# Kernel optimization log

Hardware: AMD Instinct MI355X
Metric: run time of the kernel (lower is better)

Reference implementation:

```python
import jax, jax.numpy as jnp
import numpy as np

T, B, D = 200, 1024, 128
T_OBS = 140
L = 20       # rec_dims: encoder latent per mean/std
LAT = 32     # latents: generative latent dim
GRU_U = 200  # gru_units
UNITS = 100  # hidden units of ODE-func / z0 nets


def _lin(key, fan_in, fan_out):
    return jax.random.normal(key, (fan_in, fan_out), jnp.float32) / jnp.sqrt(jnp.float32(fan_in))


def setup_inputs() -> dict:
    key = jax.random.key(0)
    ks = jax.random.split(key, 20)
    gin = 2 * L + 2 * D  # GRU input: (mean,std) + (data,mask)
    inp = {
        "truth": jax.random.normal(ks[0], (T, B, D), jnp.float32),
        "t": jnp.arange(T, dtype=jnp.float32),
        "obs_idx": jnp.sort(jax.random.randint(ks[1], (T_OBS,), 0, T)),
        "eps": jax.random.normal(ks[2], (B, LAT), jnp.float32),
        # encoder ODE func (rec_layers=1 hidden layer of UNITS)
        "enc_w1": _lin(ks[3], L, UNITS), "enc_b1": jnp.zeros(UNITS, jnp.float32),
        "enc_w2": _lin(ks[4], UNITS, L), "enc_b2": jnp.zeros(L, jnp.float32),
        # GRU unit: update / reset / new-state nets
        "gru_uw1": _lin(ks[5], gin, GRU_U), "gru_ub1": jnp.zeros(GRU_U, jnp.float32),
        "gru_uw2": _lin(ks[6], GRU_U, 2 * L), "gru_ub2": jnp.zeros(2 * L, jnp.float32),
        "gru_rw1": _lin(ks[7], gin, GRU_U), "gru_rb1": jnp.zeros(GRU_U, jnp.float32),
        "gru_rw2": _lin(ks[8], GRU_U, 2 * L), "gru_rb2": jnp.zeros(2 * L, jnp.float32),
        "gru_nw1": _lin(ks[9], gin, GRU_U), "gru_nb1": jnp.zeros(GRU_U, jnp.float32),
        "gru_nw2": _lin(ks[10], GRU_U, 2 * L), "gru_nb2": jnp.zeros(2 * L, jnp.float32),
        # transform hidden -> z0 (mean,std)
        "z0_w1": _lin(ks[11], 2 * L, UNITS), "z0_b1": jnp.zeros(UNITS, jnp.float32),
        "z0_w2": _lin(ks[12], UNITS, 2 * LAT), "z0_b2": jnp.zeros(2 * LAT, jnp.float32),
        # decoder ODE func (gen_layers=2 hidden layers of UNITS)
        "dec_w1": _lin(ks[13], LAT, UNITS), "dec_b1": jnp.zeros(UNITS, jnp.float32),
        "dec_w2": _lin(ks[14], UNITS, UNITS), "dec_b2": jnp.zeros(UNITS, jnp.float32),
        "dec_w3": _lin(ks[15], UNITS, LAT), "dec_b3": jnp.zeros(LAT, jnp.float32),
        # readout latent -> data space
        "out_w": _lin(ks[16], LAT, D), "out_b": jnp.zeros(D, jnp.float32),
    }
    return inp


def _rk4(f, y, dt):
    k1 = f(y)
    k2 = f(y + 0.5 * dt * k1)
    k3 = f(y + 0.5 * dt * k2)
    k4 = f(y + dt * k3)
    return y + (dt / 6.0) * (k1 + 2.0 * k2 + 2.0 * k3 + k4)


def reference(truth, t, obs_idx, eps,
              enc_w1, enc_b1, enc_w2, enc_b2,
              gru_uw1, gru_ub1, gru_uw2, gru_ub2,
              gru_rw1, gru_rb1, gru_rw2, gru_rb2,
              gru_nw1, gru_nb1, gru_nw2, gru_nb2,
              z0_w1, z0_b1, z0_w2, z0_b2,
              dec_w1, dec_b1, dec_w2, dec_b2, dec_w3, dec_b3,
              out_w, out_b):
    enc_f = lambda y: jnp.tanh(y @ enc_w1 + enc_b1) @ enc_w2 + enc_b2
    dec_f = lambda z: (jnp.tanh(jnp.tanh(z @ dec_w1 + dec_b1) @ dec_w2 + dec_b2)
                       @ dec_w3 + dec_b3)

    # ----- ODE-RNN encoder, run_backwards=True over observed timesteps -----
    x_obs = truth[obs_idx][::-1]                     # [To, B, D], time-reversed
    t_obs = t[obs_idx][::-1]
    dts = jnp.concatenate([jnp.zeros(1, t.dtype), jnp.diff(t_obs)])  # <=0 steps

    def enc_step(carry, inp):
        ym, ys = carry                               # [B,L] each
        x, dt = inp
        ym = _rk4(enc_f, ym, dt)                     # evolve mean between obs
        xm = jnp.concatenate([x, jnp.ones_like(x)], -1)   # data + mask(=1)
        y = jnp.concatenate([ym, ys], -1)            # [B, 2L]
        yc = jnp.concatenate([y, xm], -1)            # [B, 2L+2D]
        u = jax.nn.sigmoid(jnp.tanh(yc @ gru_uw1 + gru_ub1) @ gru_uw2 + gru_ub2)
        r = jax.nn.sigmoid(jnp.tanh(yc @ gru_rw1 + gru_rb1) @ gru_rw2 + gru_rb2)
        nc = jnp.concatenate([y * r, xm], -1)
        ns = jnp.tanh(nc @ gru_nw1 + gru_nb1) @ gru_nw2 + gru_nb2
        nm, nsd = ns[:, :L], jnp.abs(ns[:, L:])
        new_y = (1.0 - u) * jnp.concatenate([nm, nsd], -1) + u * y
        return (new_y[:, :L], new_y[:, L:]), None

    nb = truth.shape[1]
    init = (jnp.zeros((nb, L), truth.dtype), jnp.zeros((nb, L), truth.dtype))
    (ym, ys), _ = jax.lax.scan(enc_step, init, (x_obs, dts))

    # ----- z0 posterior and sample (n_traj_samples=1) -----
    h = jnp.tanh(jnp.concatenate([ym, ys], -1) @ z0_w1 + z0_b1) @ z0_w2 + z0_b2
    z0_mean, z0_std = h[:, :LAT], jnp.abs(h[:, LAT:])
    z = z0_mean + eps * z0_std                       # [B, LAT]

    # ----- Neural ODE decoder over time_steps_to_predict = t -----
    def dec_step(zc, dt):
        zn = _rk4(dec_f, zc, dt)
        return zn, zn
    _, zs = jax.lax.scan(dec_step, z, jnp.diff(t))
    sol = jnp.concatenate([z[None], zs], 0)          # [T, B, LAT]

    out = sol @ out_w + out_b                        # [T, B, D]
    return jnp.transpose(out, (1, 0, 2))[None]       # [1, B, T, D]
```

## Files before the change

### kernel.cpp

```cpp
#include <hip/hip_runtime.h>
#include <math.h>

#define BB 1024
#define DD 128
#define NWG 256
#define CH 28
#define NCH 5

#define WS_WPACK 0
#define WS_B1E   81920
#define WS_W1Y   82560
#define WS_Y     106560
#define WS_Z     147520
#define WS_HPRE  180288
#define WS_SOL   180288

__device__ __forceinline__ float bcast(float v, int lane) {
    return __uint_as_float(__builtin_amdgcn_readlane(__float_as_uint(v), lane));
}

__device__ __forceinline__ float tanh_fast(float x) {
    const float t = __builtin_amdgcn_exp2f(x * 2.88539008177793f);
    return 1.f - 2.f * __builtin_amdgcn_rcpf(t + 1.f);
}
__device__ __forceinline__ float sigm_fast(float x) {
    const float t = __builtin_amdgcn_exp2f(x * -1.4426950408889634f);
    return __builtin_amdgcn_rcpf(1.f + t);
}

__global__ __launch_bounds__(256) void prep_kernel(
    const float* __restrict__ uw1, const float* __restrict__ ub1,
    const float* __restrict__ rw1, const float* __restrict__ rb1,
    const float* __restrict__ nw1, const float* __restrict__ nb1,
    float* __restrict__ ws)
{
    int tid = blockIdx.x * blockDim.x + threadIdx.x;
    int nth = gridDim.x * blockDim.x;
    for (int idx = tid; idx < 128 * 640; idx += nth) {
        int k = idx / 640, j = idx - k * 640;
        float v = 0.f;
        if (j < 600) {
            int g = j / 200, jj = j - g * 200;
            const float* w1 = (g == 0) ? uw1 : (g == 1) ? rw1 : nw1;
            v = w1[(40 + k) * 200 + jj];
        }
        ws[WS_WPACK + idx] = v;
    }
    for (int j = tid; j < 640; j += nth) {
        float s = 0.f;
        if (j < 600) {
            int g = j / 200, jj = j - g * 200;
            const float* w1 = (g == 0) ? uw1 : (g == 1) ? rw1 : nw1;
            const float* b1 = (g == 0) ? ub1 : (g == 1) ? rb1 : nb1;
            s = b1[jj];
            for (int k = 168; k < 296; ++k) s += w1[k * 200 + jj];
        }
        ws[WS_B1E + j] = s;
    }
    for (int idx = tid; idx < 40 * 600; idx += nth) {
        int k = idx / 600, j = idx - k * 600;
        int g = j / 200, jj = j - g * 200;
        const float* w1 = (g == 0) ? uw1 : (g == 1) ? rw1 : nw1;
        ws[WS_W1Y + idx] = w1[k * 200 + jj];
    }
}

__global__ __launch_bounds__(256) void hpre_gemm(
    const float* __restrict__ truth, const int* __restrict__ obs_idx,
    const float* __restrict__ ws, float* __restrict__ hpre, int s0)
{
    __shared__ float sx[64][68];
    __shared__ float sw[64][132];
    const int t0 = threadIdx.x;
    const int jt = blockIdx.x % 5;
    const int bt = (blockIdx.x / 5) % 16;
    const int sl = blockIdx.x / 80;
    const int oi = obs_idx[139 - (s0 + sl)];
    const int b0 = bt * 64;
    const float* wpack = ws + WS_WPACK;
    const float* b1e   = ws + WS_B1E;

    const int jj  = t0 & 15;
    const int bb4 = t0 >> 4;
    float acc[8][4];
#pragma unroll
    for (int m = 0; m < 8; ++m)
#pragma unroll
        for (int q = 0; q < 4; ++q) acc[m][q] = 0.f;

    for (int kh = 0; kh < 2; ++kh) {
        __syncthreads();
        for (int i = t0; i < 64 * 16; i += 256) {
            int bb = i >> 4, kq = i & 15;
            const float4 v = *(const float4*)&truth[((size_t)oi * BB + b0 + bb) * DD + kh * 64 + kq * 4];
            *(float4*)&sx[bb][kq * 4] = v;
        }
        for (int i = t0; i < 64 * 32; i += 256) {
            int kk = i >> 5, jq = i & 31;
            const float4 v = *(const float4*)&wpack[(kh * 64 + kk) * 640 + jt * 128 + jq * 4];
            *(float4*)&sw[kk][jq * 4] = v;
        }
        __syncthreads();
#pragma unroll 4
        for (int k = 0; k < 64; ++k) {
            float xv[4], wv[8];
#pragma unroll
            for (int q = 0; q < 4; ++q) xv[q] = sx[bb4 * 4 + q][k];
#pragma unroll
            for (int m = 0; m < 8; ++m) wv[m] = sw[k][jj + 16 * m];
#pragma unroll
            for (int m = 0; m < 8; ++m)
#pragma unroll
                for (int q = 0; q < 4; ++q) acc[m][q] += wv[m] * xv[q];
        }
    }
    const int bblk = bt * 16 + bb4;
#pragma unroll
    for (int m = 0; m < 8; ++m) {
        int j = jt * 128 + jj + 16 * m;
        if (j < 600) {
            float be = b1e[j];
#pragma unroll
            for (int q = 0; q < 4; ++q)
                hpre[(size_t)((sl * 256 + bblk) * 4 + q) * 600 + j] = acc[m][q] + be;
        }
    }
}

__global__ __launch_bounds__(256, 1) void enc_chunk(
    const float* __restrict__ tg, const int* __restrict__ obs_idx,
    const float* __restrict__ eps,
    const float* __restrict__ ew1, const float* __restrict__ eb1,
    const float* __restrict__ ew2, const float* __restrict__ eb2,
    const float* __restrict__ uw2, const float* __restrict__ ub2,
    const float* __restrict__ rw2, const float* __restrict__ rb2,
    const float* __restrict__ nw2, const float* __restrict__ nb2,
    const float* __restrict__ z0w1, const float* __restrict__ z0b1,
    const float* __restrict__ z0w2, const float* __restrict__ z0b2,
    float* __restrict__ ws, int s0)
{
    __shared__ float s_t[200];
    __shared__ int   s_oi[140];
    __shared__ __align__(16) float s_y[40][4];
    __shared__ __align__(16) float s_ytmp[20][4];
    __shared__ float s_kacc[20][4];
    __shared__ __align__(16) float s_hid[4][104];
    __shared__ float s_pe[20][4][2];
    __shared__ __align__(16) float s_ew1t[100 * 20];
    __shared__ __align__(16) float s_w2n[40 * 212];
    __shared__ __align__(16) float s_hur[4][416];
    __shared__ __align__(16) float s_hn[4][208];
    __shared__ float s_pw[80][4][4];
    __shared__ float s_pn[40][4][4];
    __shared__ float s_u[40][4];
    __shared__ __align__(16) float s_yr[40][4];
    __shared__ float s_z0o[4][64];

    const int t0 = threadIdx.x;
    const int bblk = blockIdx.x;
    const int b0 = bblk * 4;
    const float* hpre = ws + WS_HPRE;

    float rgy[3][40];
    float rew2h[52];
    float rw2q[2][52];
    float eb1_r = 0.f, eb2_r = 0.f, bur_r = 0.f, bn_r = 0.f;

    if (t0 < 200) {
#pragma unroll
        for (int g = 0; g < 3; ++g)
#pragma unroll
            for (int k = 0; k < 40; ++k)
                rgy[g][k] = ws[WS_W1Y + k * 600 + g * 200 + t0];
    }
    if (t0 < 100) eb1_r = eb1[t0];
    if (t0 < 160) {
        const int c2 = t0 % 20, kh = t0 / 80;
#pragma unroll
        for (int i = 0; i < 52; ++i) {
            const int row = kh * 52 + i;
            rew2h[i] = (row < 100) ? ew2[row * 20 + c2] : 0.f;
        }
    }
    if (t0 < 80) eb2_r = eb2[t0 % 20];
    if (t0 < 160) {
        const int p = t0 % 20, g = (t0 / 20) % 2, kq = t0 / 40;
        const float* w2 = g ? rw2 : uw2;
#pragma unroll
        for (int j = 0; j < 2; ++j)
#pragma unroll
            for (int i = 0; i < 52; ++i) {
                const int row = kq * 52 + i;
                rw2q[j][i] = (row < 200) ? w2[row * 40 + p + 20 * j] : 0.f;
            }
        bur_r = ((t0 % 80) < 40) ? ub2[t0 % 80] : rb2[(t0 % 80) - 40];
        bn_r = nb2[t0 % 40];
    }

    for (int i = t0; i < 2000; i += 256) { int k = i / 100, c = i % 100; s_ew1t[c * 20 + k] = ew1[i]; }
    for (int i = t0; i < 40 * 212; i += 256) { int o = i / 212, k = i % 212; s_w2n[i] = (k < 200) ? nw2[k * 40 + o] : 0.f; }
    for (int i = t0; i < 200; i += 256) s_t[i] = tg[i];
    for (int i = t0; i < 140; i += 256) s_oi[i] = obs_idx[i];
    if (t0 < 160) { int k = t0 % 40, b = t0 / 40; s_y[k][b] = s0 ? ws[WS_Y + k * 1024 + b0 + b] : 0.f; }
    if (t0 < 4) {
#pragma unroll
        for (int i = 0; i < 4; ++i) s_hid[t0][100 + i] = 0.f;
#pragma unroll
        for (int i = 0; i < 8; ++i) { s_hur[t0][200 + i] = 0.f; s_hur[t0][408 + i] = 0.f; s_hn[t0][200 + i] = 0.f; }
    }
    __syncthreads();

    for (int sl = 0; sl < CH; ++sl) {
        const int s = s0 + sl;
        const int oi = s_oi[139 - s];
        const float dt = (s == 0) ? 0.f : (s_t[oi] - s_t[s_oi[140 - s]]);

        float hpu[4], hpr[4], hpn[4];
        if (t0 < 200) {
#pragma unroll
            for (int q = 0; q < 4; ++q) {
                const size_t r = (size_t)((sl * 256 + bblk) * 4 + q) * 600;
                hpu[q] = hpre[r + t0];
                hpr[q] = hpre[r + 200 + t0];
                hpn[q] = hpre[r + 400 + t0];
            }
        }

#pragma unroll 1
        for (int e = 0; e < 4; ++e) {
            if (t0 < 100) {
                const int c = t0;
                float a[4] = {eb1_r, eb1_r, eb1_r, eb1_r};
#pragma unroll
                for (int i = 0; i < 5; ++i) {
                    const float4 wv = *(const float4*)&s_ew1t[c * 20 + 4 * i];
                    const float wk[4] = {wv.x, wv.y, wv.z, wv.w};
#pragma unroll
                    for (int kk = 0; kk < 4; ++kk) {
                        const int k = 4 * i + kk;
                        const float4 yv = (e == 0) ? *(const float4*)&s_y[k][0]
                                                   : *(const float4*)&s_ytmp[k][0];
                        a[0] += wk[kk] * yv.x; a[1] += wk[kk] * yv.y;
                        a[2] += wk[kk] * yv.z; a[3] += wk[kk] * yv.w;
                    }
                }
#pragma unroll
                for (int b = 0; b < 4; ++b) s_hid[b][c] = tanh_fast(a[b]);
            }
            __syncthreads();
            if (t0 < 160) {
                const int c2 = t0 % 20, b = (t0 / 20) % 4, kh = t0 / 80;
                float acc = 0.f;
#pragma unroll
                for (int i = 0; i < 13; ++i) {
                    const float4 hv = *(const float4*)&s_hid[b][kh * 52 + 4 * i];
                    acc += hv.x * rew2h[4 * i] + hv.y * rew2h[4 * i + 1]
                         + hv.z * rew2h[4 * i + 2] + hv.w * rew2h[4 * i + 3];
                }
                s_pe[c2][b][kh] = acc;
            }
            __syncthreads();
            if (t0 < 80) {
                const int c2 = t0 % 20, b = t0 / 20;
                const float kv = eb2_r + s_pe[c2][b][0] + s_pe[c2][b][1];
                const float y0 = s_y[c2][b];
                if (e == 0)      { s_kacc[c2][b] = kv;        s_ytmp[c2][b] = y0 + 0.5f * dt * kv; }
                else if (e == 1) { s_kacc[c2][b] += 2.f * kv; s_ytmp[c2][b] = y0 + 0.5f * dt * kv; }
                else if (e == 2) { s_kacc[c2][b] += 2.f * kv; s_ytmp[c2][b] = y0 + dt * kv; }
                else             { s_y[c2][b] = y0 + (dt / 6.f) * (s_kacc[c2][b] + kv); }
            }
            __syncthreads();
        }

        if (t0 < 200) {
            float au[4], ar[4];
#pragma unroll
            for (int b = 0; b < 4; ++b) { au[b] = hpu[b]; ar[b] = hpr[b]; }
#pragma unroll
            for (int k = 0; k < 40; ++k) {
                const float4 yv = *(const float4*)&s_y[k][0];
                const float wu = rgy[0][k], wr = rgy[1][k];
                au[0] += wu * yv.x; au[1] += wu * yv.y; au[2] += wu * yv.z; au[3] += wu * yv.w;
                ar[0] += wr * yv.x; ar[1] += wr * yv.y; ar[2] += wr * yv.z; ar[3] += wr * yv.w;
            }
#pragma unroll
            for (int b = 0; b < 4; ++b) {
                s_hur[b][t0] = tanh_fast(au[b]);
                s_hur[b][208 + t0] = tanh_fast(ar[b]);
            }
        }
        __syncthreads();

        if (t0 < 160) {
            const int p = t0 % 20, g = (t0 / 20) % 2, kq = t0 / 40;
            const int goff = g * 208;
            float a1[4] = {0.f, 0.f, 0.f, 0.f}, a2[4] = {0.f, 0.f, 0.f, 0.f};
#pragma unroll
            for (int i = 0; i < 13; ++i) {
                const float wa = rw2q[0][4 * i], wb = rw2q[0][4 * i + 1],
                            wc = rw2q[0][4 * i + 2], wd = rw2q[0][4 * i + 3];
                const float we = rw2q[1][4 * i], wf = rw2q[1][4 * i + 1],
                            wg = rw2q[1][4 * i + 2], wh = rw2q[1][4 * i + 3];
#pragma unroll
                for (int b = 0; b < 4; ++b) {
                    const float4 hv = *(const float4*)&s_hur[b][goff + kq * 52 + 4 * i];
                    a1[b] += hv.x * wa + hv.y * wb + hv.z * wc + hv.w * wd;
                    a2[b] += hv.x * we + hv.y * wf + hv.z * wg + hv.w * wh;
                }
            }
            const int o1 = 40 * g + p, o2 = o1 + 20;
#pragma unroll
            for (int b = 0; b < 4; ++b) { s_pw[o1][b][kq] = a1[b]; s_pw[o2][b][kq] = a2[b]; }
        }
        __syncthreads();

        if (t0 < 160) {
            const int o = t0 % 80, bp = t0 / 80;
#pragma unroll
            for (int j = 0; j < 2; ++j) {
                const int b = 2 * bp + j;
                const float v = bur_r + s_pw[o][b][0] + s_pw[o][b][1] + s_pw[o][b][2] + s_pw[o][b][3];
                const float sg = sigm_fast(v);
                if (o < 40) s_u[o][b] = sg;
                else        s_yr[o - 40][b] = s_y[o - 40][b] * sg;
            }
        }
        __syncthreads();

        if (t0 < 200) {
            float an[4];
#pragma unroll
            for (int b = 0; b < 4; ++b) an[b] = hpn[b];
#pragma unroll
            for (int k = 0; k < 40; ++k) {
                const float4 yv = *(const float4*)&s_yr[k][0];
                const float w = rgy[2][k];
                an[0] += w * yv.x; an[1] += w * yv.y; an[2] += w * yv.z; an[3] += w * yv.w;
            }
#pragma unroll
            for (int b = 0; b < 4; ++b) s_hn[b][t0] = tanh_fast(an[b]);
        }
        __syncthreads();

        if (t0 < 160) {
            const int o = t0 % 40, kq = t0 / 40;
            float an[4] = {0.f, 0.f, 0.f, 0.f};
#pragma unroll
            for (int i = 0; i < 13; ++i) {
                const float4 wv = *(const float4*)&s_w2n[o * 212 + kq * 52 + 4 * i];
#pragma unroll
                for (int b = 0; b < 4; ++b) {
                    const float4 hv = *(const float4*)&s_hn[b][kq * 52 + 4 * i];
                    an[b] += hv.x * wv.x + hv.y * wv.y + hv.z * wv.z + hv.w * wv.w;
                }
            }
#pragma unroll
            for (int b = 0; b < 4; ++b) s_pn[o][b][kq] = an[b];
        }
        __syncthreads();

        if (t0 < 160) {
            const int o = t0 % 40, b = t0 / 40;
            const float v = bn_r + s_pn[o][b][0] + s_pn[o][b][1] + s_pn[o][b][2] + s_pn[o][b][3];
            const float cand = (o < 20) ? v : fabsf(v);
            const float uu = s_u[o][b];
            s_y[o][b] = (1.f - uu) * cand + uu * s_y[o][b];
        }
        __syncthreads();
    }

    if (s0 + CH == 140) {
        if (t0 < 100) {
            const int c = t0;
            float a[4] = {z0b1[c], z0b1[c], z0b1[c], z0b1[c]};
#pragma unroll
            for (int k = 0; k < 40; ++k) {
                const float4 yv = *(const float4*)&s_y[k][0];
                const float w = z0w1[k * 100 + c];
                a[0] += w * yv.x; a[1] += w * yv.y; a[2] += w * yv.z; a[3] += w * yv.w;
            }
#pragma unroll
            for (int b = 0; b < 4; ++b) s_hid[b][c] = tanh_fast(a[b]);
        }
        __syncthreads();
        {
            const int b = t0 / 64, u = t0 % 64;
            float acc = z0b2[u];
#pragma unroll
            for (int i = 0; i < 25; ++i) {
                const float4 hv = *(const float4*)&s_hid[b][4 * i];
                acc += hv.x * z0w2[(4 * i) * 64 + u] + hv.y * z0w2[(4 * i + 1) * 64 + u]
                     + hv.z * z0w2[(4 * i + 2) * 64 + u] + hv.w * z0w2[(4 * i + 3) * 64 + u];
            }
            s_z0o[b][u] = acc;
        }
        __syncthreads();
        if (t0 < 128) {
            const int b = t0 / 32, i = t0 % 32;
            const int gb = b0 + b;
            ws[WS_Z + gb * 32 + i] = s_z0o[b][i] + eps[gb * 32 + i] * fabsf(s_z0o[b][32 + i]);
        }
    }
    if (t0 < 160) {
        const int k = t0 % 40, b = t0 / 40;
        ws[WS_Y + k * 1024 + b0 + b] = s_y[k][b];
    }
}

__global__ __launch_bounds__(128, 2) void dec_kernel(
    const float* __restrict__ tg,
    const float* __restrict__ dw1, const float* __restrict__ db1,
    const float* __restrict__ dw2, const float* __restrict__ db2,
    const float* __restrict__ dw3, const float* __restrict__ db3,
    float* __restrict__ ws)
{
    __shared__ float s_t[200];
    __shared__ float s_p1[2][100];
    __shared__ float s_p2[2][100];
    __shared__ float s_p3[2][32];

    const int t0 = threadIdx.x;
    const int w  = t0 >> 6;
    const int l  = t0 & 63;
    const int batch = blockIdx.x;

    const int c0 = l;
    const int c1 = 64 + l;
    const bool has1 = (l < 36);
    const int j3 = l & 31;

    float rw1a[16], rw1b[16], rw2a[50], rw2b[50], rw3[50];
#pragma unroll
    for (int i = 0; i < 16; ++i) {
        rw1a[i] = dw1[(16 * w + i) * 100 + c0];
        rw1b[i] = has1 ? dw1[(16 * w + i) * 100 + c1] : 0.f;
    }
#pragma unroll
    for (int i = 0; i < 50; ++i) {
        rw2a[i] = dw2[(50 * w + i) * 100 + c0];
        rw2b[i] = has1 ? dw2[(50 * w + i) * 100 + c1] : 0.f;
        rw3[i]  = dw3[(50 * w + i) * 32 + j3];
    }
    const float rb1a = db1[c0];
    const float rb1b = has1 ? db1[c1] : 0.f;
    const float rb2a = db2[c0];
    const float rb2b = has1 ? db2[c1] : 0.f;
    const float rb3  = db3[j3];

    for (int i = t0; i < 200; i += 128) s_t[i] = tg[i];

    float z_r = ws[WS_Z + (size_t)batch * 32 + j3];
    __syncthreads();

    float zs = z_r, ka_r = 0.f;

    for (int s = 0; s < 200; ++s) {
        if (t0 < 32)
            ws[WS_SOL + (size_t)(s * 1024 + batch) * 32 + l] = z_r;
        if (s == 199) break;
        const float dtv = s_t[s + 1] - s_t[s];

#pragma unroll 1
        for (int e = 0; e < 4; ++e) {
            float a0 = 0.f, a1 = 0.f;
            if (w == 0) {
#pragma unroll
                for (int i = 0; i < 16; ++i) {
                    const float sv = bcast(zs, i);
                    a0 += sv * rw1a[i]; a1 += sv * rw1b[i];
                }
            } else {
#pragma unroll
                for (int i = 0; i < 16; ++i) {
                    const float sv = bcast(zs, 16 + i);
                    a0 += sv * rw1a[i]; a1 += sv * rw1b[i];
                }
            }
            s_p1[w][c0] = a0;
            if (has1) s_p1[w][c1] = a1;
            __syncthreads();
            const float h1_0 = tanh_fast(rb1a + a0 + s_p1[w ^ 1][c0]);
            const float h1_1 = has1 ? tanh_fast(rb1b + a1 + s_p1[w ^ 1][c1]) : 0.f;

            float a2 = 0.f, a3 = 0.f;
            if (w == 0) {
#pragma unroll
                for (int i = 0; i < 50; ++i) {
                    const float sv = bcast(h1_0, i);
                    a2 += sv * rw2a[i]; a3 += sv * rw2b[i];
                }
            } else {
#pragma unroll
                for (int i = 0; i < 14; ++i) {
                    const float sv = bcast(h1_0, 50 + i);
                    a2 += sv * rw2a[i]; a3 += sv * rw2b[i];
                }
#pragma unroll
                for (int i = 14; i < 50; ++i) {
                    const float sv = bcast(h1_1, i - 14);
                    a2 += sv * rw2a[i]; a3 += sv * rw2b[i];
                }
            }
            s_p2[w][c0] = a2;
            if (has1) s_p2[w][c1] = a3;
            __syncthreads();
            const float h2_0 = tanh_fast(rb2a + a2 + s_p2[w ^ 1][c0]);
            const float h2_1 = has1 ? tanh_fast(rb2b + a3 + s_p2[w ^ 1][c1]) : 0.f;

            float ap = 0.f;
            if (w == 0) {
#pragma unroll
                for (int i = 0; i < 50; ++i) ap += bcast(h2_0, i) * rw3[i];
            } else {
#pragma unroll
                for (int i = 0; i < 14; ++i) ap += bcast(h2_0, 50 + i) * rw3[i];
#pragma unroll
                for (int i = 14; i < 50; ++i) ap += bcast(h2_1, i - 14) * rw3[i];
            }
            if (l < 32) s_p3[w][l] = ap;
            __syncthreads();
            const float kj = rb3 + s_p3[0][j3] + s_p3[1][j3];

            if (e == 0)      { ka_r = kj;        zs = z_r + 0.5f * dtv * kj; }
            else if (e == 1) { ka_r += 2.f * kj; zs = z_r + 0.5f * dtv * kj; }
            else if (e == 2) { ka_r += 2.f * kj; zs = z_r + dtv * kj; }
            else             { z_r += (dtv / 6.f) * (ka_r + kj); zs = z_r; }
        }
    }
}

__global__ __launch_bounds__(256) void proj_kernel(
    const float* __restrict__ ow, const float* __restrict__ ob,
    const float* __restrict__ ws, float* __restrict__ out)
{
    const int t0 = threadIdx.x;
    const int d = t0 & 127, half = t0 >> 7;
    float rw[32];
#pragma unroll
    for (int k = 0; k < 32; ++k) rw[k] = ow[k * 128 + d];
    const float bo = ob[d];
    const int sb0 = blockIdx.x * 64 + half * 32;
#pragma unroll 2
    for (int m = 0; m < 32; ++m) {
        const int sb = sb0 + m;
        const int s = sb >> 10, b = sb & 1023;
        const float4* zp = (const float4*)&ws[WS_SOL + (size_t)sb * 32];
        float acc = bo;
#pragma unroll
        for (int kq = 0; kq < 8; ++kq) {
            const float4 zv = zp[kq];
            acc += zv.x * rw[4 * kq] + zv.y * rw[4 * kq + 1]
                 + zv.z * rw[4 * kq + 2] + zv.w * rw[4 * kq + 3];
        }
        out[((size_t)b * 200 + s) * 128 + d] = acc;
    }
}

extern "C" void kernel_launch(void* const* d_in, const int* in_sizes, int n_in,
                              void* d_out, int out_size, void* d_ws, size_t ws_size,
                              hipStream_t stream)
{
    const float* truth = (const float*)d_in[0];
    const float* tg    = (const float*)d_in[1];
    const int*   oi    = (const int*)d_in[2];
    const float* eps   = (const float*)d_in[3];
    const float* ew1   = (const float*)d_in[4];
    const float* eb1   = (const float*)d_in[5];
    const float* ew2   = (const float*)d_in[6];
    const float* eb2   = (const float*)d_in[7];
    const float* uw1   = (const float*)d_in[8];
    const float* ub1   = (const float*)d_in[9];
    const float* uw2   = (const float*)d_in[10];
    const float* ub2   = (const float*)d_in[11];
    const float* rw1   = (const float*)d_in[12];
    const float* rb1   = (const float*)d_in[13];
    const float* rw2   = (const float*)d_in[14];
    const float* rb2   = (const float*)d_in[15];
    const float* nw1   = (const float*)d_in[16];
    const float* nb1   = (const float*)d_in[17];
    const float* nw2   = (const float*)d_in[18];
    const float* nb2   = (const float*)d_in[19];
    const float* z0w1  = (const float*)d_in[20];
    const float* z0b1  = (const float*)d_in[21];
    const float* z0w2  = (const float*)d_in[22];
    const float* z0b2  = (const float*)d_in[23];
    const float* dw1   = (const float*)d_in[24];
    const float* db1   = (const float*)d_in[25];
    const float* dw2   = (const float*)d_in[26];
    const float* db2   = (const float*)d_in[27];
    const float* dw3   = (const float*)d_in[28];
    const float* db3   = (const float*)d_in[29];
    const float* ow    = (const float*)d_in[30];
    const float* ob    = (const float*)d_in[31];
    float* ws  = (float*)d_ws;
    float* out = (float*)d_out;

    prep_kernel<<<dim3(120), dim3(256), 0, stream>>>(uw1, ub1, rw1, rb1, nw1, nb1, ws);
    for (int c = 0; c < NCH; ++c) {
        hpre_gemm<<<dim3(CH * 16 * 5), dim3(256), 0, stream>>>(truth, oi, ws, ws + WS_HPRE, c * CH);
        enc_chunk<<<dim3(NWG), dim3(256), 0, stream>>>(
            tg, oi, eps, ew1, eb1, ew2, eb2, uw2, ub2, rw2, rb2, nw2, nb2,
            z0w1, z0b1, z0w2, z0b2, ws, c * CH);
    }
    dec_kernel<<<dim3(1024), dim3(128), 0, stream>>>(tg, dw1, db1, dw2, db2, dw3, db3, ws);
    proj_kernel<<<dim3(3200), dim3(256), 0, stream>>>(ow, ob, ws, out);
}
```

Baseline: 3.800 ms.

## Cut encoder register pressure to allow two workgroups per CU

Raises enc_chunk launch bounds to two workgroups per CU. To fit the register budget, it moves the encoder ODE second-layer weights from per-thread registers into a transposed, padded shared-memory array. It also defers the hpre loads from the top of each step to just before their use. This frees registers for higher occupancy, but adds LDS traffic and exposes global-load latency that was previously hidden behind the RK4 loop.

```diff
diff --git a/kernel.cpp b/kernel.cpp
--- a/kernel.cpp
+++ b/kernel.cpp
@@ -127,7 +127,7 @@
     }
 }
 
-__global__ __launch_bounds__(256, 1) void enc_chunk(
+__global__ __launch_bounds__(256, 2) void enc_chunk(
     const float* __restrict__ tg, const int* __restrict__ obs_idx,
     const float* __restrict__ eps,
     const float* __restrict__ ew1, const float* __restrict__ eb1,
@@ -147,6 +147,7 @@
     __shared__ __align__(16) float s_hid[4][104];
     __shared__ float s_pe[20][4][2];
     __shared__ __align__(16) float s_ew1t[100 * 20];
+    __shared__ __align__(16) float s_ew2t[20 * 108];
     __shared__ __align__(16) float s_w2n[40 * 212];
     __shared__ __align__(16) float s_hur[4][416];
     __shared__ __align__(16) float s_hn[4][208];
@@ -162,7 +163,6 @@
     const float* hpre = ws + WS_HPRE;
 
     float rgy[3][40];
-    float rew2h[52];
     float rw2q[2][52];
     float eb1_r = 0.f, eb2_r = 0.f, bur_r = 0.f, bn_r = 0.f;
 
@@ -174,14 +174,6 @@
                 rgy[g][k] = ws[WS_W1Y + k * 600 + g * 200 + t0];
     }
     if (t0 < 100) eb1_r = eb1[t0];
-    if (t0 < 160) {
-        const int c2 = t0 % 20, kh = t0 / 80;
-#pragma unroll
-        for (int i = 0; i < 52; ++i) {
-            const int row = kh * 52 + i;
-            rew2h[i] = (row < 100) ? ew2[row * 20 + c2] : 0.f;
-        }
-    }
     if (t0 < 80) eb2_r = eb2[t0 % 20];
     if (t0 < 160) {
         const int p = t0 % 20, g = (t0 / 20) % 2, kq = t0 / 40;
@@ -198,6 +190,8 @@
     }
 
     for (int i = t0; i < 2000; i += 256) { int k = i / 100, c = i % 100; s_ew1t[c * 20 + k] = ew1[i]; }
+    for (int i = t0; i < 2000; i += 256) { int row = i / 20, c = i % 20; s_ew2t[c * 108 + row] = ew2[i]; }
+    if (t0 < 160) { int c = t0 % 20, r = 100 + t0 / 20; s_ew2t[c * 108 + r] = 0.f; }
     for (int i = t0; i < 40 * 212; i += 256) { int o = i / 212, k = i % 212; s_w2n[i] = (k < 200) ? nw2[k * 40 + o] : 0.f; }
     for (int i = t0; i < 200; i += 256) s_t[i] = tg[i];
     for (int i = t0; i < 140; i += 256) s_oi[i] = obs_idx[i];
@@ -214,17 +208,6 @@
         const int s = s0 + sl;
         const int oi = s_oi[139 - s];
         const float dt = (s == 0) ? 0.f : (s_t[oi] - s_t[s_oi[140 - s]]);
-
-        float hpu[4], hpr[4], hpn[4];
-        if (t0 < 200) {
-#pragma unroll
-            for (int q = 0; q < 4; ++q) {
-                const size_t r = (size_t)((sl * 256 + bblk) * 4 + q) * 600;
-                hpu[q] = hpre[r + t0];
-                hpr[q] = hpre[r + 200 + t0];
-                hpn[q] = hpre[r + 400 + t0];
-            }
-        }
 
 #pragma unroll 1
         for (int e = 0; e < 4; ++e) {
@@ -250,12 +233,13 @@
             __syncthreads();
             if (t0 < 160) {
                 const int c2 = t0 % 20, b = (t0 / 20) % 4, kh = t0 / 80;
+                const float* wp = &s_ew2t[c2 * 108 + kh * 52];
                 float acc = 0.f;
 #pragma unroll
                 for (int i = 0; i < 13; ++i) {
+                    const float4 wv = *(const float4*)&wp[4 * i];
                     const float4 hv = *(const float4*)&s_hid[b][kh * 52 + 4 * i];
-                    acc += hv.x * rew2h[4 * i] + hv.y * rew2h[4 * i + 1]
-                         + hv.z * rew2h[4 * i + 2] + hv.w * rew2h[4 * i + 3];
+                    acc += hv.x * wv.x + hv.y * wv.y + hv.z * wv.z + hv.w * wv.w;
                 }
                 s_pe[c2][b][kh] = acc;
             }
@@ -275,7 +259,11 @@
         if (t0 < 200) {
             float au[4], ar[4];
 #pragma unroll
-            for (int b = 0; b < 4; ++b) { au[b] = hpu[b]; ar[b] = hpr[b]; }
+            for (int q = 0; q < 4; ++q) {
+                const size_t r = (size_t)((sl * 256 + bblk) * 4 + q) * 600;
+                au[q] = hpre[r + t0];
+                ar[q] = hpre[r + 200 + t0];
+            }
 #pragma unroll
             for (int k = 0; k < 40; ++k) {
                 const float4 yv = *(const float4*)&s_y[k][0];
@@ -330,7 +318,10 @@
         if (t0 < 200) {
             float an[4];
 #pragma unroll
-            for (int b = 0; b < 4; ++b) an[b] = hpn[b];
+            for (int q = 0; q < 4; ++q) {
+                const size_t r = (size_t)((sl * 256 + bblk) * 4 + q) * 600;
+                an[q] = hpre[r + 400 + t0];
+            }
 #pragma unroll
             for (int k = 0; k < 40; ++k) {
                 const float4 yv = *(const float4*)&s_yr[k][0];
```

New measurement: 4.639 ms. 22.1% more time.
